# Kernel tuning notes

Hardware: AMD Instinct MI355X
Metric: run time of the kernel (lower is better)

The kernel has to match this reference:

```python
import jax, jax.numpy as jnp
import numpy as np

D_MODEL = 1024
D_STATE = 64
BATCH = 4
SEQ_L = 4096
LN_EPS = 1e-5


def setup_inputs() -> dict:
    key = jax.random.key(0)
    ks = jax.random.split(key, 8)
    u = jax.random.normal(ks[0], (BATCH, SEQ_L, D_MODEL), jnp.float32)
    # Parameters mirroring StateSpaceLayer._initialize_parameters
    A_log = jax.random.uniform(ks[1], (D_STATE,), jnp.float32, -2.0, -0.1)
    xav = float(np.sqrt(6.0 / (D_STATE + D_MODEL)))
    B = jax.random.uniform(ks[2], (D_STATE, D_MODEL), jnp.float32, -xav, xav) * 0.1
    C = jax.random.uniform(ks[3], (D_MODEL, D_STATE), jnp.float32, -xav, xav) * 0.1
    D = jnp.zeros((D_MODEL,), jnp.float32)
    delta = jax.random.uniform(ks[4], (D_MODEL,), jnp.float32, 0.001, 0.1)
    gamma = jnp.ones((D_MODEL,), jnp.float32)
    beta = jnp.zeros((D_MODEL,), jnp.float32)
    freq_align = jax.random.normal(ks[5], (D_MODEL,), jnp.float32)
    reward = jax.random.normal(ks[6], (D_MODEL,), jnp.float32)
    return dict(u=u, A_log=A_log, B=B, C=C, D=D, delta=delta,
                gamma=gamma, beta=beta, freq_align=freq_align, reward=reward)


def reference(u, A_log, B, C, D, delta, gamma, beta, freq_align, reward):
    b, L, d = u.shape
    A = -jnp.exp(A_log)                                   # [N]
    # --- convolution kernel: K[k] = C @ (A_bar[0])^k, A_bar[0] = exp(delta[0]*A) ---
    k_idx = jnp.arange(L, dtype=u.dtype)                  # [L]
    powers = jnp.exp(k_idx[:, None] * (delta[0] * A)[None, :])  # [L, N]
    K = jnp.einsum('ln,dn->ld', powers, C)                # [L, D]
    # --- FFT-based causal (circular, zero-padded) convolution ---
    fft_size = 1 << int(np.ceil(np.log2(2 * L)))
    u_fft = jnp.fft.fft(u, n=fft_size, axis=1)            # [B, F, D] complex
    K_fft = jnp.fft.fft(K, n=fft_size, axis=0)            # [F, D] complex
    y = jnp.fft.ifft(u_fft * K_fft[None], axis=1).real[:, :L, :]
    # --- D skip connection ---
    y = y + u * D
    # --- FFT-based learning signals: scale spectrum, add real 'reward' to every bin ---
    y_fft = jnp.fft.fft(y, axis=1)
    y = jnp.fft.ifft(y_fft * freq_align + reward, axis=1).real
    # --- LayerNorm (eval-mode dropout = identity) ---
    mean = y.mean(-1, keepdims=True)
    var = y.var(-1, keepdims=True)
    y = (y - mean) / jnp.sqrt(var + LN_EPS) * gamma + beta
    # --- final state update with mean timescale ---
    delta_mean = delta.mean()
    A_bar_s = jnp.exp(delta_mean * A)                     # [N]
    A_safe = A + 1e-8 * jnp.sign(A)
    B_bar = ((A_bar_s - 1.0) / A_safe)[:, None] * B       # [N, D]
    state = jnp.zeros((b, A.shape[0]), u.dtype)
    final_state = A_bar_s * state + jnp.einsum('nd,bd->bn', B_bar, u[:, -1, :])
    return (y, final_state)
```

## Files before the change

### kernel.cpp

```cpp
#include <hip/hip_runtime.h>
#include <math.h>

#define BATCH  4
#define SEQL   4096
#define DMODEL 1024
#define NSTATE 64
#define LN_EPS 1e-5f
#define TB     16

typedef unsigned short u16;
typedef unsigned int   u32;
typedef float f32x2 __attribute__((ext_vector_type(2)));

__device__ __forceinline__ f32x2 fma2(f32x2 a, f32x2 b, f32x2 c) {
#if __has_builtin(__builtin_elementwise_fma)
    return __builtin_elementwise_fma(a, b, c);
#else
    f32x2 d; d.x = fmaf(a.x, b.x, c.x); d.y = fmaf(a.y, b.y, c.y); return d;
#endif
}

__device__ __forceinline__ u16 f2bf(float x) {
    u32 b = __float_as_uint(x);
    b += 0x7FFF + ((b >> 16) & 1);
    return (u16)(b >> 16);
}
__device__ __forceinline__ float bf2f(u16 h) {
    return __uint_as_float(((u32)h) << 16);
}

__global__ __launch_bounds__(256) void k_local(const float* __restrict__ u,
                                               const float* __restrict__ A_log,
                                               const float* __restrict__ delta,
                                               u16* __restrict__ f,
                                               int NCH, int TCH) {
    __shared__ float r_lds[NSTATE];
    const int tid = threadIdx.x;
    const int w = tid >> 6, l = tid & 63;
    const int b   = blockIdx.x / (16 * NCH);
    const int rem = blockIdx.x % (16 * NCH);
    const int dt  = rem / NCH;
    const int j   = rem % NCH;
    const int n0  = w << 4;
    const int d   = (dt << 6) | l;

    if (tid < NSTATE) r_lds[tid] = expf(delta[0] * -expf(A_log[tid]));
    __syncthreads();

    f32x2 r2[8], s2[8];
#pragma unroll
    for (int p = 0; p < 8; ++p) {
        r2[p] = *(const f32x2*)&r_lds[n0 + 2 * p];
        s2[p] = (f32x2)(0.f, 0.f);
    }

    const float* ub = u + ((size_t)b * SEQL + (size_t)j * TCH) * DMODEL + d;
    for (int tb = 0; tb < TCH / TB; ++tb) {
        float ur[TB];
#pragma unroll
        for (int t = 0; t < TB; ++t)
            ur[t] = ub[(size_t)(tb * TB + t) * DMODEL];
#pragma unroll
        for (int q = 0; q < 4; ++q) {
            f32x2 sa = s2[2*q], sb = s2[2*q+1];
            const f32x2 ra = r2[2*q], rb = r2[2*q+1];
#pragma unroll
            for (int t = 0; t < TB; ++t) {
                f32x2 u2; u2.x = ur[t]; u2.y = ur[t];
                sa = fma2(ra, sa, u2);
                sb = fma2(rb, sb, u2);
            }
            s2[2*q] = sa; s2[2*q+1] = sb;
        }
    }
    u16* fb = f + (((size_t)b * NCH + j) * NSTATE + n0) * DMODEL + d;
#pragma unroll
    for (int p = 0; p < 8; ++p) {
        fb[(size_t)(2*p)     * DMODEL] = f2bf(s2[p].x);
        fb[(size_t)(2*p + 1) * DMODEL] = f2bf(s2[p].y);
    }
}

__global__ __launch_bounds__(256) void k_pass2(const float* __restrict__ A_log,
                                               const float* __restrict__ delta,
                                               u16* __restrict__ f,
                                               int NCH, int TCH) {
    const int tid = blockIdx.x * 256 + threadIdx.x;
    const int d = tid & (DMODEL - 1);
    const int n = (tid >> 10) & (NSTATE - 1);
    const int b = tid >> 16;
    const float A  = -expf(A_log[n]);
    const float rT = expf((float)TCH * delta[0] * A);
    float I = 0.f;
    u16* p = f + ((size_t)b * NCH * NSTATE + n) * DMODEL + d;
    const size_t stride = (size_t)NSTATE * DMODEL;
    for (int j = 0; j < NCH; ++j) {
        float tmp = bf2f(p[(size_t)j * stride]);
        p[(size_t)j * stride] = f2bf(I);
        I = fmaf(rT, I, tmp);
    }
}

template <bool ZBF16>
__global__ __launch_bounds__(256) void k_replay(const float* __restrict__ u,
                                                const float* __restrict__ A_log,
                                                const float* __restrict__ C,
                                                const float* __restrict__ Dvec,
                                                const float* __restrict__ delta,
                                                const u16* __restrict__ I,
                                                const float* __restrict__ fal,
                                                const float* __restrict__ rw,
                                                void* __restrict__ zout,
                                                int NCH, int TCH) {
    __shared__ float r_lds[NSTATE];
    __shared__ float part[2][4][TB][64];
    const int tid = threadIdx.x;
    const int w = tid >> 6, l = tid & 63;
    const int b   = blockIdx.x / (16 * NCH);
    const int rem = blockIdx.x % (16 * NCH);
    const int dt  = rem / NCH;
    const int j   = rem % NCH;
    const int n0  = w << 4;
    const int d   = (dt << 6) | l;

    if (tid < NSTATE) r_lds[tid] = expf(delta[0] * -expf(A_log[tid]));
    __syncthreads();

    const float fad = fal[d];
    f32x2 r2[8], c2[8], s2[8];
#pragma unroll
    for (int p = 0; p < 8; ++p)
        r2[p] = *(const f32x2*)&r_lds[n0 + 2 * p];
#pragma unroll
    for (int p = 0; p < 8; ++p) {
        c2[p].x = fad * C[(size_t)d * NSTATE + n0 + 2*p];
        c2[p].y = fad * C[(size_t)d * NSTATE + n0 + 2*p + 1];
    }
    const u16* Ib = I + (((size_t)b * NCH + j) * NSTATE + n0) * DMODEL + d;
#pragma unroll
    for (int p = 0; p < 8; ++p) {
        s2[p].x = bf2f(Ib[(size_t)(2*p)     * DMODEL]);
        s2[p].y = bf2f(Ib[(size_t)(2*p + 1) * DMODEL]);
    }

    const float Ddf = Dvec[d] * fad;
    const float rwd = rw[d];
    const float* ub = u + ((size_t)b * SEQL + (size_t)j * TCH) * DMODEL + d;
    const size_t zoff = ((size_t)b * SEQL + (size_t)j * TCH) * DMODEL + d;
    u16*   zb16 = (u16*)zout + zoff;
    float* zb32 = (float*)zout + zoff;

    for (int tb = 0; tb < TCH / TB; ++tb) {
        const int pb = tb & 1;
        float ur[TB];
        f32x2 zr2[TB];
#pragma unroll
        for (int t = 0; t < TB; ++t) {
            ur[t] = ub[(size_t)(tb * TB + t) * DMODEL];
            zr2[t] = (f32x2)(0.f, 0.f);
        }
#pragma unroll
        for (int q = 0; q < 4; ++q) {
            f32x2 sa = s2[2*q], sb = s2[2*q+1];
            const f32x2 ra = r2[2*q], rb = r2[2*q+1];
            const f32x2 ca = c2[2*q], cb = c2[2*q+1];
#pragma unroll
            for (int t = 0; t < TB; ++t) {
                f32x2 u2; u2.x = ur[t]; u2.y = ur[t];
                sa = fma2(ra, sa, u2);
                sb = fma2(rb, sb, u2);
                zr2[t] = fma2(ca, sa, zr2[t]);
                zr2[t] = fma2(cb, sb, zr2[t]);
            }
            s2[2*q] = sa; s2[2*q+1] = sb;
        }
#pragma unroll
        for (int t = 0; t < TB; ++t) {
            float v = zr2[t].x + zr2[t].y;
            if (w == 0) v = fmaf(Ddf, ur[t], v);
            part[pb][w][t][l] = v;
        }
        __syncthreads();
#pragma unroll
        for (int k = 0; k < 4; ++k) {
            const int t = (w << 2) | k;
            float v = (part[pb][0][t][l] + part[pb][1][t][l]) +
                      (part[pb][2][t][l] + part[pb][3][t][l]);
            if (j == 0 && tb == 0 && t == 0) v += rwd;
            if (ZBF16) zb16[(size_t)(tb * TB + t) * DMODEL] = f2bf(v);
            else       zb32[(size_t)(tb * TB + t) * DMODEL] = v;
        }
    }
}

template <bool ZBF16>
__global__ __launch_bounds__(256) void k_ln(const void* __restrict__ zin,
                                            float* __restrict__ y,
                                            const float* __restrict__ gamma,
                                            const float* __restrict__ beta) {
    const int tid = threadIdx.x;
    float4 v;
    if (ZBF16) {
        const ushort4 h = ((const ushort4*)((const u16*)zin + (size_t)blockIdx.x * DMODEL))[tid];
        v.x = bf2f(h.x); v.y = bf2f(h.y); v.z = bf2f(h.z); v.w = bf2f(h.w);
    } else {
        v = ((const float4*)((const float*)zin + (size_t)blockIdx.x * DMODEL))[tid];
    }
    float sum = v.x + v.y + v.z + v.w;
    float sq  = v.x*v.x + v.y*v.y + v.z*v.z + v.w*v.w;
#pragma unroll
    for (int off = 32; off > 0; off >>= 1) {
        sum += __shfl_down(sum, off, 64);
        sq  += __shfl_down(sq,  off, 64);
    }
    __shared__ float red[8];
    const int wave = tid >> 6, lane = tid & 63;
    if (lane == 0) { red[wave] = sum; red[4 + wave] = sq; }
    __syncthreads();
    sum = red[0] + red[1] + red[2] + red[3];
    sq  = red[4] + red[5] + red[6] + red[7];
    const float mean = sum * (1.f / DMODEL);
    const float var  = sq * (1.f / DMODEL) - mean * mean;
    const float inv  = 1.f / sqrtf(var + LN_EPS);
    const float4 g  = ((const float4*)gamma)[tid];
    const float4 bb = ((const float4*)beta)[tid];
    float4 o;
    o.x = (v.x - mean) * inv * g.x + bb.x;
    o.y = (v.y - mean) * inv * g.y + bb.y;
    o.z = (v.z - mean) * inv * g.z + bb.z;
    o.w = (v.w - mean) * inv * g.w + bb.w;
    ((float4*)(y + (size_t)blockIdx.x * DMODEL))[tid] = o;
}

__global__ __launch_bounds__(256) void k_state(const float* __restrict__ u,
                                               const float* __restrict__ A_log,
                                               const float* __restrict__ B,
                                               const float* __restrict__ delta,
                                               float* __restrict__ out) {
    const int n = blockIdx.x & 63;
    const int b = blockIdx.x >> 6;
    const int tid = threadIdx.x;
    const float* ul = u + ((size_t)b * SEQL + (SEQL - 1)) * DMODEL;
    const float* Bn = B + (size_t)n * DMODEL;
    float dot = 0.f, dsum = 0.f;
    for (int dd = tid; dd < DMODEL; dd += 256) {
        dot = fmaf(Bn[dd], ul[dd], dot);
        dsum += delta[dd];
    }
#pragma unroll
    for (int off = 32; off > 0; off >>= 1) {
        dot  += __shfl_down(dot,  off, 64);
        dsum += __shfl_down(dsum, off, 64);
    }
    __shared__ float red[8];
    const int wave = tid >> 6, lane = tid & 63;
    if (lane == 0) { red[wave] = dot; red[4 + wave] = dsum; }
    __syncthreads();
    if (tid == 0) {
        dot  = red[0] + red[1] + red[2] + red[3];
        dsum = red[4] + red[5] + red[6] + red[7];
        const float dmean = dsum * (1.f / DMODEL);
        const float A = -expf(A_log[n]);
        const float Abar = expf(dmean * A);
        const float Asafe = A + (A >= 0.f ? 1e-8f : -1e-8f);
        out[blockIdx.x] = ((Abar - 1.f) / Asafe) * dot;
    }
}

extern "C" void kernel_launch(void* const* d_in, const int* in_sizes, int n_in,
                              void* d_out, int out_size, void* d_ws, size_t ws_size,
                              hipStream_t stream) {
    const float* u     = (const float*)d_in[0];
    const float* A_log = (const float*)d_in[1];
    const float* B     = (const float*)d_in[2];
    const float* C     = (const float*)d_in[3];
    const float* Dv    = (const float*)d_in[4];
    const float* delta = (const float*)d_in[5];
    const float* gamma = (const float*)d_in[6];
    const float* beta  = (const float*)d_in[7];
    const float* fal   = (const float*)d_in[8];
    const float* rw    = (const float*)d_in[9];

    float* y  = (float*)d_out;
    float* st = y + (size_t)BATCH * SEQL * DMODEL;
    u16* f    = (u16*)d_ws;

    int NCH = 16;
    while (NCH > 4 && (size_t)BATCH * NCH * NSTATE * DMODEL * sizeof(u16) > ws_size)
        NCH >>= 1;
    const int TCH = SEQL / NCH;
    const int nb = BATCH * 16 * NCH;

    const size_t f_bytes = (size_t)BATCH * NCH * NSTATE * DMODEL * sizeof(u16);
    const size_t z_bytes = (size_t)BATCH * SEQL * DMODEL * sizeof(u16);
    const bool zbf16 = (f_bytes + z_bytes) <= ws_size;
    void* zbuf = zbf16 ? (void*)((char*)d_ws + f_bytes) : (void*)y;

    hipLaunchKernelGGL(k_local, dim3(nb), dim3(256), 0, stream, u, A_log, delta, f, NCH, TCH);
    hipLaunchKernelGGL(k_pass2, dim3(BATCH * NSTATE * DMODEL / 256), dim3(256), 0, stream,
                       A_log, delta, f, NCH, TCH);
    if (zbf16) {
        hipLaunchKernelGGL((k_replay<true>), dim3(nb), dim3(256), 0, stream,
                           u, A_log, C, Dv, delta, f, fal, rw, zbuf, NCH, TCH);
        hipLaunchKernelGGL((k_ln<true>), dim3(BATCH * SEQL), dim3(256), 0, stream,
                           zbuf, y, gamma, beta);
    } else {
        hipLaunchKernelGGL((k_replay<false>), dim3(nb), dim3(256), 0, stream,
                           u, A_log, C, Dv, delta, f, fal, rw, zbuf, NCH, TCH);
        hipLaunchKernelGGL((k_ln<false>), dim3(BATCH * SEQL), dim3(256), 0, stream,
                           zbuf, y, gamma, beta);
    }
    hipLaunchKernelGGL(k_state, dim3(BATCH * NSTATE), dim3(256), 0, stream,
                       u, A_log, B, delta, st);
}
```

Before: 123.0 us.

## Fold chunk-prefix scan into replay kernel and merge state kernel into local pass

```diff
diff --git a/kernel.cpp b/kernel.cpp
--- a/kernel.cpp
+++ b/kernel.cpp
@@ -29,11 +29,45 @@
     return __uint_as_float(((u32)h) << 16);
 }
 
-__global__ __launch_bounds__(256) void k_local(const float* __restrict__ u,
-                                               const float* __restrict__ A_log,
-                                               const float* __restrict__ delta,
-                                               u16* __restrict__ f,
-                                               int NCH, int TCH) {
+__global__ __launch_bounds__(256) void k_local_state(const float* __restrict__ u,
+                                                     const float* __restrict__ A_log,
+                                                     const float* __restrict__ delta,
+                                                     const float* __restrict__ Bm,
+                                                     u16* __restrict__ f,
+                                                     float* __restrict__ st,
+                                                     int NCH, int TCH, int nb) {
+    if (blockIdx.x >= nb) {
+        const int sb = blockIdx.x - nb;
+        const int n = sb & 63;
+        const int b = sb >> 6;
+        const int tid = threadIdx.x;
+        const float* ul = u + ((size_t)b * SEQL + (SEQL - 1)) * DMODEL;
+        const float* Bn = Bm + (size_t)n * DMODEL;
+        float dot = 0.f, dsum = 0.f;
+        for (int dd = tid; dd < DMODEL; dd += 256) {
+            dot = fmaf(Bn[dd], ul[dd], dot);
+            dsum += delta[dd];
+        }
+#pragma unroll
+        for (int off = 32; off > 0; off >>= 1) {
+            dot  += __shfl_down(dot,  off, 64);
+            dsum += __shfl_down(dsum, off, 64);
+        }
+        __shared__ float red[8];
+        const int wave = tid >> 6, lane = tid & 63;
+        if (lane == 0) { red[wave] = dot; red[4 + wave] = dsum; }
+        __syncthreads();
+        if (tid == 0) {
+            dot  = red[0] + red[1] + red[2] + red[3];
+            dsum = red[4] + red[5] + red[6] + red[7];
+            const float dmean = dsum * (1.f / DMODEL);
+            const float A = -expf(A_log[n]);
+            const float Abar = expf(dmean * A);
+            const float Asafe = A + (A >= 0.f ? 1e-8f : -1e-8f);
+            st[sb] = ((Abar - 1.f) / Asafe) * dot;
+        }
+        return;
+    }
     __shared__ float r_lds[NSTATE];
     const int tid = threadIdx.x;
     const int w = tid >> 6, l = tid & 63;
@@ -62,15 +96,15 @@
             ur[t] = ub[(size_t)(tb * TB + t) * DMODEL];
 #pragma unroll
         for (int q = 0; q < 4; ++q) {
-            f32x2 sa = s2[2*q], sb = s2[2*q+1];
+            f32x2 sa = s2[2*q], sb2 = s2[2*q+1];
             const f32x2 ra = r2[2*q], rb = r2[2*q+1];
 #pragma unroll
             for (int t = 0; t < TB; ++t) {
                 f32x2 u2; u2.x = ur[t]; u2.y = ur[t];
-                sa = fma2(ra, sa, u2);
-                sb = fma2(rb, sb, u2);
+                sa  = fma2(ra, sa,  u2);
+                sb2 = fma2(rb, sb2, u2);
             }
-            s2[2*q] = sa; s2[2*q+1] = sb;
+            s2[2*q] = sa; s2[2*q+1] = sb2;
         }
     }
     u16* fb = f + (((size_t)b * NCH + j) * NSTATE + n0) * DMODEL + d;
@@ -78,26 +112,6 @@
     for (int p = 0; p < 8; ++p) {
         fb[(size_t)(2*p)     * DMODEL] = f2bf(s2[p].x);
         fb[(size_t)(2*p + 1) * DMODEL] = f2bf(s2[p].y);
-    }
-}
-
-__global__ __launch_bounds__(256) void k_pass2(const float* __restrict__ A_log,
-                                               const float* __restrict__ delta,
-                                               u16* __restrict__ f,
-                                               int NCH, int TCH) {
-    const int tid = blockIdx.x * 256 + threadIdx.x;
-    const int d = tid & (DMODEL - 1);
-    const int n = (tid >> 10) & (NSTATE - 1);
-    const int b = tid >> 16;
-    const float A  = -expf(A_log[n]);
-    const float rT = expf((float)TCH * delta[0] * A);
-    float I = 0.f;
-    u16* p = f + ((size_t)b * NCH * NSTATE + n) * DMODEL + d;
-    const size_t stride = (size_t)NSTATE * DMODEL;
-    for (int j = 0; j < NCH; ++j) {
-        float tmp = bf2f(p[(size_t)j * stride]);
-        p[(size_t)j * stride] = f2bf(I);
-        I = fmaf(rT, I, tmp);
     }
 }
 
@@ -107,12 +121,13 @@
                                                 const float* __restrict__ C,
                                                 const float* __restrict__ Dvec,
                                                 const float* __restrict__ delta,
-                                                const u16* __restrict__ I,
+                                                const u16* __restrict__ f,
                                                 const float* __restrict__ fal,
                                                 const float* __restrict__ rw,
                                                 void* __restrict__ zout,
                                                 int NCH, int TCH) {
     __shared__ float r_lds[NSTATE];
+    __shared__ float rT_lds[NSTATE];
     __shared__ float part[2][4][TB][64];
     const int tid = threadIdx.x;
     const int w = tid >> 6, l = tid & 63;
@@ -123,24 +138,45 @@
     const int n0  = w << 4;
     const int d   = (dt << 6) | l;
 
-    if (tid < NSTATE) r_lds[tid] = expf(delta[0] * -expf(A_log[tid]));
+    if (tid < NSTATE) {
+        const float A = -expf(A_log[tid]);
+        const float d0v = delta[0];
+        r_lds[tid]  = expf(d0v * A);
+        rT_lds[tid] = expf((float)TCH * d0v * A);
+    }
     __syncthreads();
 
     const float fad = fal[d];
     f32x2 r2[8], c2[8], s2[8];
 #pragma unroll
-    for (int p = 0; p < 8; ++p)
+    for (int p = 0; p < 8; ++p) {
         r2[p] = *(const f32x2*)&r_lds[n0 + 2 * p];
+        s2[p] = (f32x2)(0.f, 0.f);
+    }
 #pragma unroll
     for (int p = 0; p < 8; ++p) {
         c2[p].x = fad * C[(size_t)d * NSTATE + n0 + 2*p];
         c2[p].y = fad * C[(size_t)d * NSTATE + n0 + 2*p + 1];
     }
-    const u16* Ib = I + (((size_t)b * NCH + j) * NSTATE + n0) * DMODEL + d;
-#pragma unroll
-    for (int p = 0; p < 8; ++p) {
-        s2[p].x = bf2f(Ib[(size_t)(2*p)     * DMODEL]);
-        s2[p].y = bf2f(Ib[(size_t)(2*p + 1) * DMODEL]);
+
+    {
+        f32x2 rT2[8];
+#pragma unroll
+        for (int p = 0; p < 8; ++p)
+            rT2[p] = *(const f32x2*)&rT_lds[n0 + 2 * p];
+        const u16* fbase = f + ((size_t)b * NCH * NSTATE + n0) * DMODEL + d;
+        const size_t kstride = (size_t)NSTATE * DMODEL;
+#pragma unroll 1
+        for (int k = 0; k < j; ++k) {
+            const u16* fk = fbase + (size_t)k * kstride;
+#pragma unroll
+            for (int p = 0; p < 8; ++p) {
+                f32x2 fv;
+                fv.x = bf2f(fk[(size_t)(2*p)     * DMODEL]);
+                fv.y = bf2f(fk[(size_t)(2*p + 1) * DMODEL]);
+                s2[p] = fma2(rT2[p], s2[p], fv);
+            }
+        }
     }
 
     const float Ddf = Dvec[d] * fad;
@@ -161,18 +197,18 @@
         }
 #pragma unroll
         for (int q = 0; q < 4; ++q) {
-            f32x2 sa = s2[2*q], sb = s2[2*q+1];
+            f32x2 sa = s2[2*q], sb2 = s2[2*q+1];
             const f32x2 ra = r2[2*q], rb = r2[2*q+1];
             const f32x2 ca = c2[2*q], cb = c2[2*q+1];
 #pragma unroll
             for (int t = 0; t < TB; ++t) {
                 f32x2 u2; u2.x = ur[t]; u2.y = ur[t];
-                sa = fma2(ra, sa, u2);
-                sb = fma2(rb, sb, u2);
-                zr2[t] = fma2(ca, sa, zr2[t]);
-                zr2[t] = fma2(cb, sb, zr2[t]);
+                sa  = fma2(ra, sa,  u2);
+                sb2 = fma2(rb, sb2, u2);
+                zr2[t] = fma2(ca, sa,  zr2[t]);
+                zr2[t] = fma2(cb, sb2, zr2[t]);
             }
-            s2[2*q] = sa; s2[2*q+1] = sb;
+            s2[2*q] = sa; s2[2*q+1] = sb2;
         }
 #pragma unroll
         for (int t = 0; t < TB; ++t) {
@@ -232,41 +268,6 @@
     ((float4*)(y + (size_t)blockIdx.x * DMODEL))[tid] = o;
 }
 
-__global__ __launch_bounds__(256) void k_state(const float* __restrict__ u,
-                                               const float* __restrict__ A_log,
-                                               const float* __restrict__ B,
-                                               const float* __restrict__ delta,
-                                               float* __restrict__ out) {
-    const int n = blockIdx.x & 63;
-    const int b = blockIdx.x >> 6;
-    const int tid = threadIdx.x;
-    const float* ul = u + ((size_t)b * SEQL + (SEQL - 1)) * DMODEL;
-    const float* Bn = B + (size_t)n * DMODEL;
-    float dot = 0.f, dsum = 0.f;
-    for (int dd = tid; dd < DMODEL; dd += 256) {
-        dot = fmaf(Bn[dd], ul[dd], dot);
-        dsum += delta[dd];
-    }
-#pragma unroll
-    for (int off = 32; off > 0; off >>= 1) {
-        dot  += __shfl_down(dot,  off, 64);
-        dsum += __shfl_down(dsum, off, 64);
-    }
-    __shared__ float red[8];
-    const int wave = tid >> 6, lane = tid & 63;
-    if (lane == 0) { red[wave] = dot; red[4 + wave] = dsum; }
-    __syncthreads();
-    if (tid == 0) {
-        dot  = red[0] + red[1] + red[2] + red[3];
-        dsum = red[4] + red[5] + red[6] + red[7];
-        const float dmean = dsum * (1.f / DMODEL);
-        const float A = -expf(A_log[n]);
-        const float Abar = expf(dmean * A);
-        const float Asafe = A + (A >= 0.f ? 1e-8f : -1e-8f);
-        out[blockIdx.x] = ((Abar - 1.f) / Asafe) * dot;
-    }
-}
-
 extern "C" void kernel_launch(void* const* d_in, const int* in_sizes, int n_in,
                               void* d_out, int out_size, void* d_ws, size_t ws_size,
                               hipStream_t stream) {
@@ -296,9 +297,8 @@
     const bool zbf16 = (f_bytes + z_bytes) <= ws_size;
     void* zbuf = zbf16 ? (void*)((char*)d_ws + f_bytes) : (void*)y;
 
-    hipLaunchKernelGGL(k_local, dim3(nb), dim3(256), 0, stream, u, A_log, delta, f, NCH, TCH);
-    hipLaunchKernelGGL(k_pass2, dim3(BATCH * NSTATE * DMODEL / 256), dim3(256), 0, stream,
-                       A_log, delta, f, NCH, TCH);
+    hipLaunchKernelGGL(k_local_state, dim3(nb + BATCH * NSTATE), dim3(256), 0, stream,
+                       u, A_log, delta, B, f, st, NCH, TCH, nb);
     if (zbf16) {
         hipLaunchKernelGGL((k_replay<true>), dim3(nb), dim3(256), 0, stream,
                            u, A_log, C, Dv, delta, f, fal, rw, zbuf, NCH, TCH);
@@ -310,6 +310,4 @@
         hipLaunchKernelGGL((k_ln<false>), dim3(BATCH * SEQL), dim3(256), 0, stream,
                            zbuf, y, gamma, beta);
     }
-    hipLaunchKernelGGL(k_state, dim3(BATCH * NSTATE), dim3(256), 0, stream,
-                       u, A_log, B, delta, st);
-}
+}
```

Result: faster. 120.2 us (-2.2%).
